# Optimization experiments

Measured on AMD Instinct MI355X. Metric: run time of the kernel, lower is better.

The kernel has to match this reference:

```python
import jax, jax.numpy as jnp
import numpy as np

K = 9
KS = (K - 1) // 2  # k_self
C_LIGHT = 299792458.0 / 1e6 / 600.0  # speed of light in detector units (as in HLayer)
BN_EPS = 1e-3  # keras BatchNormalization default epsilon


def _win2(f):
    # (B, N) -> (B, N, K): out[b, n, k] = f[b, n + k - KS], zero-padded at boundaries
    B, N = f.shape
    fp = jnp.pad(f, ((0, 0), (KS, KS)))
    return jnp.stack([fp[:, k:k + N] for k in range(K)], axis=2)


def _win3(f):
    # (B, N, F) -> (B, N, K, F): same shift-window along N
    B, N, F = f.shape
    fp = jnp.pad(f, ((0, 0), (KS, KS), (0, 0)))
    return jnp.stack([fp[:, k:k + N, :] for k in range(K)], axis=2)


def _valid_mask(N):
    # (N, K): True where neighbor index n + k - KS is in range
    idx = jnp.arange(N)[:, None] + jnp.arange(K)[None, :] - KS
    return (idx >= 0) & (idx < N)


def _hlayer(x):
    # x: (B, N, 6) with cols (t, c, a, px, py, pz) -> (B, N, K, 12)
    t, c, a = x[..., 0], x[..., 1], x[..., 2]
    px, py, pz = x[..., 3], x[..., 4], x[..., 5]
    N = x.shape[1]
    valid = _valid_mask(N)[None, :, :]  # (1, N, K)

    def d(f):  # shifted minus self, zeroed at boundaries (matches TF pad of the diff)
        return jnp.where(valid, _win2(f) - f[:, :, None], 0.0)

    dt, dx, dy, dz = d(t), d(px), d(py), d(pz)
    eu2 = dx * dx + dy * dy + dz * dz
    euclidean = jnp.sqrt(eu2)
    lorentz = (C_LIGHT * dt) ** 2 - eu2
    feats = [_win2(t), _win2(px), _win2(py), _win2(pz), _win2(c), _win2(a),
             dt, dx, dy, dz, euclidean, lorentz]
    return jnp.stack(feats, axis=3)  # (B, N, K, 12)


def _conv_bn(x, W, b, gamma, beta, mean, var):
    # kernel-size-1 Conv1D with relu activation, then inference-mode BatchNorm
    y = jax.nn.relu(jnp.matmul(x, W) + b)
    return gamma * (y - mean) * jax.lax.rsqrt(var + BN_EPS) + beta


def _make_params(key, dims):
    params = {}
    for i, (fi, fo) in enumerate(zip(dims[:-1], dims[1:])):
        key, k1 = jax.random.split(key)
        s = np.sqrt(2.0 / fi)
        params[f'W{i}'] = jax.random.normal(k1, (fi, fo), jnp.float32) * s
        params[f'b{i}'] = jnp.zeros((fo,), jnp.float32)
        key, k2, k3, k4 = jax.random.split(key, 4)
        params[f'g{i}'] = 1.0 + 0.1 * jax.random.normal(k2, (fo,), jnp.float32)
        params[f'be{i}'] = 0.1 * jax.random.normal(k3, (fo,), jnp.float32)
        params[f'mu{i}'] = 0.1 * jax.random.normal(k4, (fo,), jnp.float32)
        params[f'var{i}'] = 0.5 + jax.random.uniform(key, (fo,), jnp.float32)
    return params


def setup_inputs() -> dict:
    key = jax.random.key(0)
    kx, km, kf = jax.random.split(key, 3)
    B, N = 8, 4096
    x = jax.random.normal(kx, (B, N, 6), jnp.float32)
    dims_m = [12, 128, 256]   # MLayer/CRLayer stack on H features
    dims_f = [6, 128, 256]    # FRLayer stack on raw inputs
    pm = _make_params(km, dims_m)
    pf = _make_params(kf, dims_f)
    inp = {'x': x}
    for i in range(2):
        for n in ['W', 'b', 'g', 'be', 'mu', 'var']:
            inp[f'm_{n}{i}'] = pm[f'{n}{i}']
            inp[f'f_{n}{i}'] = pf[f'{n}{i}']
    return inp


def reference(x,
              m_W0, m_b0, m_g0, m_be0, m_mu0, m_var0,
              m_W1, m_b1, m_g1, m_be1, m_mu1, m_var1,
              f_W0, f_b0, f_g0, f_be0, f_mu0, f_var0,
              f_W1, f_b1, f_g1, f_be1, f_mu1, f_var1):
    # H-layer: (B, N, 6) -> (B, N, K, 12) geometric neighbor features
    h = _hlayer(x)
    # M branch (CRLayer, 1x1 convs over feature dim): -> m_nkf (B, N, K, 256)
    m = _conv_bn(h, m_W0, m_b0, m_g0, m_be0, m_mu0, m_var0)
    m = _conv_bn(m, m_W1, m_b1, m_g1, m_be1, m_mu1, m_var1)
    # FR branch on raw inputs: -> fr_nf (B, N, 256)
    fr = _conv_bn(x, f_W0, f_b0, f_g0, f_be0, f_mu0, f_var0)
    fr = _conv_bn(fr, f_W1, f_b1, f_g1, f_be1, f_mu1, f_var1)
    # A-layer: gate shifted fr by m and max-aggregate over K neighbors
    fr_sh = _win3(fr)                      # (B, N, K, 256), zero-padded shifts
    T = m * fr_sh                          # (B, N, K, 256)
    return jnp.max(T, axis=2)              # (B, N, 256)
```

## Files before the change

### kernel.cpp

```cpp
#include <hip/hip_runtime.h>
#include <hip/hip_bf16.h>

#define N_PTS 4096
#define C_LIGHT 0.49965409666666664f
#define BN_EPS 1e-3f

typedef __attribute__((ext_vector_type(8))) short short8;
typedef __attribute__((ext_vector_type(4))) float f32x4;

static __device__ __forceinline__ unsigned short f2bf(float f) {
    unsigned u = __float_as_uint(f);
    u += 0x7FFFu + ((u >> 16) & 1u);
    return (unsigned short)(u >> 16);
}
static __device__ __forceinline__ float bf2f(unsigned short h) {
    return __uint_as_float(((unsigned)h) << 16);
}
static __device__ __forceinline__ unsigned pk2(float a, float b) {
    __hip_bfloat162 h = __float22bfloat162_rn(make_float2(a, b));
    union { __hip_bfloat162 v; unsigned u; } cv;
    cv.v = h;
    return cv.u;
}

__global__ __launch_bounds__(256) void fold_kernel(
    const float* __restrict__ mW1, const float* __restrict__ mb1,
    const float* __restrict__ mg0, const float* __restrict__ mbe0,
    const float* __restrict__ mmu0, const float* __restrict__ mvar0,
    const float* __restrict__ mg1, const float* __restrict__ mbe1,
    const float* __restrict__ mmu1, const float* __restrict__ mvar1,
    const float* __restrict__ fW1p, const float* __restrict__ fb1,
    const float* __restrict__ fg0, const float* __restrict__ fbe0,
    const float* __restrict__ fmu0, const float* __restrict__ fvar0,
    const float* __restrict__ fg1, const float* __restrict__ fbe1,
    const float* __restrict__ fmu1, const float* __restrict__ fvar1,
    float* __restrict__ mBf, float* __restrict__ mS1, float* __restrict__ mT1,
    unsigned short* __restrict__ mWhi, unsigned short* __restrict__ mWlo,
    float* __restrict__ fBf, float* __restrict__ fS1, float* __restrict__ fT1,
    unsigned short* __restrict__ fWhi, unsigned short* __restrict__ fWlo)
{
    int br = blockIdx.x;
    const float* W1  = br ? fW1p : mW1;
    const float* b1  = br ? fb1  : mb1;
    const float* g0  = br ? fg0  : mg0;
    const float* be0 = br ? fbe0 : mbe0;
    const float* mu0 = br ? fmu0 : mmu0;
    const float* var0= br ? fvar0: mvar0;
    const float* g1  = br ? fg1  : mg1;
    const float* be1 = br ? fbe1 : mbe1;
    const float* mu1 = br ? fmu1 : mmu1;
    const float* var1= br ? fvar1: mvar1;
    float* Bf = br ? fBf : mBf;
    float* S1 = br ? fS1 : mS1;
    float* T1 = br ? fT1 : mT1;
    unsigned short* Whi = br ? fWhi : mWhi;
    unsigned short* Wlo = br ? fWlo : mWlo;

    __shared__ float s0s[128], t0s[128];
    int t = threadIdx.x;
    if (t < 128) {
        float s = g0[t] / sqrtf(var0[t] + BN_EPS);
        s0s[t] = s;
        t0s[t] = be0[t] - mu0[t] * s;
    }
    __syncthreads();

    {
        float s1 = g1[t] / sqrtf(var1[t] + BN_EPS);
        S1[t] = s1;
        T1[t] = be1[t] - mu1[t] * s1;
        float acc = b1[t];
        for (int i = 0; i < 128; ++i) acc = fmaf(t0s[i], W1[i * 256 + t], acc);
        Bf[t] = acc;
    }

    for (int e = t; e < 32768; e += 256) {
        int j = e & 7, l = (e >> 3) & 63, ks = (e >> 9) & 3, ct = e >> 11;
        int i = ks * 32 + (l >> 4) * 8 + j;
        int c = ct * 16 + (l & 15);
        float w = s0s[i] * W1[i * 256 + c];
        unsigned short hi = f2bf(w);
        unsigned short lo = f2bf(w - bf2f(hi));
        Whi[e] = hi;
        Wlo[e] = lo;
    }
}

__global__ __launch_bounds__(256, 2) void fr_kernel(
    const float* __restrict__ x,
    const float* __restrict__ W0,
    const float* __restrict__ b0,
    const short8* __restrict__ WfHi, const short8* __restrict__ WfLo,
    const float* __restrict__ Bf, const float* __restrict__ S1,
    const float* __restrict__ T1,
    float* __restrict__ frT)
{
    __shared__ float xs[64][6];
    __shared__ __attribute__((aligned(16))) float w0s[6][136];
    __shared__ __attribute__((aligned(16))) float b0s[128];
    __shared__ __attribute__((aligned(16))) unsigned short hAhi[4 * 64 * 8];
    __shared__ __attribute__((aligned(16))) unsigned short hAlo[4 * 64 * 8];

    int t = threadIdx.x;
    long row0 = (long)blockIdx.x * 64;

    for (int i = t; i < 384; i += 256) xs[i / 6][i % 6] = x[row0 * 6 + i];
    for (int i = t; i < 768; i += 256) w0s[i >> 7][i & 127] = W0[i];
    if (t < 128) b0s[t] = b0[t];

    int lane = t & 63, wv = t >> 6;
    int laneN = lane & 15, laneH = lane >> 4;
    int cg = t & 7;

    float bfv[4], s1v[4], t1v[4];
    int colc[4];
#pragma unroll
    for (int c = 0; c < 4; ++c) {
        colc[c] = (wv * 4 + c) * 16 + laneN;
        bfv[c] = Bf[colc[c]];
        s1v[c] = S1[colc[c]];
        t1v[c] = T1[colc[c]];
    }
    f32x4 acc[4][4];
#pragma unroll
    for (int mt = 0; mt < 4; ++mt)
#pragma unroll
        for (int c = 0; c < 4; ++c) {
            f32x4 z = {bfv[c], bfv[c], bfv[c], bfv[c]};
            acc[mt][c] = z;
        }
    __syncthreads();

    for (int ks = 0; ks < 4; ++ks) {
        int k0 = ks * 32 + cg * 4;
        float4 wreg[6];
#pragma unroll
        for (int i = 0; i < 6; ++i) wreg[i] = *(const float4*)&w0s[i][k0];
        float4 bq = *(const float4*)&b0s[k0];

        for (int idx = t; idx < 512; idx += 256) {
            int row = idx >> 3;
            float a0 = bq.x, a1 = bq.y, a2 = bq.z, a3 = bq.w;
#pragma unroll
            for (int i = 0; i < 6; ++i) {
                float hv = xs[row][i];
                a0 = fmaf(hv, wreg[i].x, a0);
                a1 = fmaf(hv, wreg[i].y, a1);
                a2 = fmaf(hv, wreg[i].z, a2);
                a3 = fmaf(hv, wreg[i].w, a3);
            }
            a0 = fmaxf(a0, 0.f); a1 = fmaxf(a1, 0.f);
            a2 = fmaxf(a2, 0.f); a3 = fmaxf(a3, 0.f);
            unsigned hi01 = pk2(a0, a1), hi23 = pk2(a2, a3);
            float q0 = __uint_as_float(hi01 << 16);
            float q1 = __uint_as_float(hi01 & 0xffff0000u);
            float q2 = __uint_as_float(hi23 << 16);
            float q3 = __uint_as_float(hi23 & 0xffff0000u);
            unsigned lo01 = pk2(a0 - q0, a1 - q1), lo23 = pk2(a2 - q2, a3 - q3);
            int mt = row >> 4, nl = row & 15;
            int base = (mt * 64 + (cg >> 1) * 16 + nl) * 8 + (cg & 1) * 4;
            *(uint2*)&hAhi[base] = make_uint2(hi01, hi23);
            *(uint2*)&hAlo[base] = make_uint2(lo01, lo23);
        }
        __syncthreads();

        short8 Bhi[4], Blo[4];
#pragma unroll
        for (int c = 0; c < 4; ++c) {
            int fo = ((wv * 4 + c) * 4 + ks) * 64 + lane;
            Bhi[c] = WfHi[fo];
            Blo[c] = WfLo[fo];
        }
#pragma unroll
        for (int mt = 0; mt < 4; ++mt) {
            short8 Ahi = *(const short8*)&hAhi[(mt * 64 + lane) * 8];
            short8 Alo = *(const short8*)&hAlo[(mt * 64 + lane) * 8];
#pragma unroll
            for (int c = 0; c < 4; ++c) {
                f32x4 a = acc[mt][c];
                a = __builtin_amdgcn_mfma_f32_16x16x32_bf16(Alo, Bhi[c], a, 0, 0, 0);
                a = __builtin_amdgcn_mfma_f32_16x16x32_bf16(Ahi, Blo[c], a, 0, 0, 0);
                a = __builtin_amdgcn_mfma_f32_16x16x32_bf16(Ahi, Bhi[c], a, 0, 0, 0);
                acc[mt][c] = a;
            }
        }
        __syncthreads();
    }

#pragma unroll
    for (int c = 0; c < 4; ++c)
#pragma unroll
        for (int mt = 0; mt < 4; ++mt) {
            float4 o;
            o.x = fmaf(fmaxf(acc[mt][c][0], 0.f), s1v[c], t1v[c]);
            o.y = fmaf(fmaxf(acc[mt][c][1], 0.f), s1v[c], t1v[c]);
            o.z = fmaf(fmaxf(acc[mt][c][2], 0.f), s1v[c], t1v[c]);
            o.w = fmaf(fmaxf(acc[mt][c][3], 0.f), s1v[c], t1v[c]);
            *(float4*)&frT[(long)colc[c] * 32768 + row0 + mt * 16 + laneH * 4] = o;
        }
}

#define SM_XS   0
#define SM_B0   576
#define SM_W0   1088
#define SM_HF   7616
#define SM_AHI  14528
#define SM_ALO  23744
#define SM_FRT  0
#define SM_OUT  33792
#define SM_TOT  50432

__global__ __launch_bounds__(256, 2) void fused_kernel(
    const float* __restrict__ x,
    const float* __restrict__ W0,
    const float* __restrict__ b0,
    const short8* __restrict__ WfHi, const short8* __restrict__ WfLo,
    const float* __restrict__ Bf, const float* __restrict__ S1,
    const float* __restrict__ T1,
    const float* __restrict__ frT,
    float* __restrict__ out)
{
    __shared__ __attribute__((aligned(16))) char smem[SM_TOT];
    float* xs  = (float*)(smem + SM_XS);
    float* b0s = (float*)(smem + SM_B0);
    float* w0s = (float*)(smem + SM_W0);
    float* hfp = (float*)(smem + SM_HF);
    unsigned short* hAhi = (unsigned short*)(smem + SM_AHI);
    unsigned short* hAlo = (unsigned short*)(smem + SM_ALO);
    float* frL = (float*)(smem + SM_FRT);
    float* oL  = (float*)(smem + SM_OUT);

    int t = threadIdx.x;
    int bn = blockIdx.x;
    int b  = bn >> 8;
    int n0 = (bn & 255) << 4;
    const float* xb = x + (long)b * N_PTS * 6;

    if (t < 144) {
        int rr = t / 6, cc = t % 6;
        int n = n0 - 4 + rr;
        xs[rr * 6 + cc] = (n >= 0 && n < N_PTS) ? xb[n * 6 + cc] : 0.f;
    }
    for (int i = t; i < 12 * 128; i += 256) w0s[(i >> 7) * 136 + (i & 127)] = W0[i];
    if (t < 128) b0s[t] = b0[t];
    __syncthreads();

    if (t < 144) {
        int kt = t >> 4, nl = t & 15;
        const float* self = &xs[(nl + 4) * 6];
        const float* nb   = &xs[(nl + kt) * 6];
        int nbn = n0 + nl + kt - 4;
        float msk = (nbn >= 0 && nbn < N_PTS) ? 1.f : 0.f;
        float dt = (nb[0] - self[0]) * msk;
        float dx = (nb[3] - self[3]) * msk;
        float dy = (nb[4] - self[4]) * msk;
        float dz = (nb[5] - self[5]) * msk;
        float eu2 = dx * dx + dy * dy + dz * dz;
        float* h = &hfp[t * 12];
        h[0]  = nb[0];
        h[1]  = nb[3];
        h[2]  = nb[4];
        h[3]  = nb[5];
        h[4]  = nb[1];
        h[5]  = nb[2];
        h[6]  = dt;
        h[7]  = dx;
        h[8]  = dy;
        h[9]  = dz;
        h[10] = sqrtf(eu2);
        float cdt = C_LIGHT * dt;
        h[11] = cdt * cdt - eu2;
    }

    int lane = t & 63, wv = t >> 6;
    int laneN = lane & 15, laneH = lane >> 4;
    int cg = t & 7;

    float bfv[4], s1v[4], t1v[4];
    int colc[4];
#pragma unroll
    for (int c = 0; c < 4; ++c) {
        colc[c] = (wv * 4 + c) * 16 + laneN;
        bfv[c] = Bf[colc[c]];
        s1v[c] = S1[colc[c]];
        t1v[c] = T1[colc[c]];
    }
    f32x4 acc[9][4];
#pragma unroll
    for (int kt = 0; kt < 9; ++kt)
#pragma unroll
        for (int c = 0; c < 4; ++c) {
            f32x4 z = {bfv[c], bfv[c], bfv[c], bfv[c]};
            acc[kt][c] = z;
        }
    __syncthreads();

    for (int ks = 0; ks < 4; ++ks) {
        int k0 = ks * 32 + cg * 4;
        float4 wreg[12];
#pragma unroll
        for (int i = 0; i < 12; ++i) wreg[i] = *(const float4*)&w0s[i * 136 + k0];
        float4 bq = *(const float4*)&b0s[k0];

        for (int idx = t; idx < 1152; idx += 256) {
            int row = idx >> 3;
            float a0 = bq.x, a1 = bq.y, a2 = bq.z, a3 = bq.w;
#pragma unroll
            for (int i = 0; i < 12; ++i) {
                float hv = hfp[row * 12 + i];
                a0 = fmaf(hv, wreg[i].x, a0);
                a1 = fmaf(hv, wreg[i].y, a1);
                a2 = fmaf(hv, wreg[i].z, a2);
                a3 = fmaf(hv, wreg[i].w, a3);
            }
            a0 = fmaxf(a0, 0.f); a1 = fmaxf(a1, 0.f);
            a2 = fmaxf(a2, 0.f); a3 = fmaxf(a3, 0.f);
            unsigned hi01 = pk2(a0, a1), hi23 = pk2(a2, a3);
            float q0 = __uint_as_float(hi01 << 16);
            float q1 = __uint_as_float(hi01 & 0xffff0000u);
            float q2 = __uint_as_float(hi23 << 16);
            float q3 = __uint_as_float(hi23 & 0xffff0000u);
            unsigned lo01 = pk2(a0 - q0, a1 - q1), lo23 = pk2(a2 - q2, a3 - q3);
            int kt = row >> 4, nl = row & 15;
            int base = (kt * 64 + (cg >> 1) * 16 + nl) * 8 + (cg & 1) * 4;
            *(uint2*)&hAhi[base] = make_uint2(hi01, hi23);
            *(uint2*)&hAlo[base] = make_uint2(lo01, lo23);
        }
        __syncthreads();

        short8 Bhi[4], Blo[4];
#pragma unroll
        for (int c = 0; c < 4; ++c) {
            int fo = ((wv * 4 + c) * 4 + ks) * 64 + lane;
            Bhi[c] = WfHi[fo];
            Blo[c] = WfLo[fo];
        }
#pragma unroll
        for (int kt = 0; kt < 9; ++kt) {
            short8 Ahi = *(const short8*)&hAhi[(kt * 64 + lane) * 8];
            short8 Alo = *(const short8*)&hAlo[(kt * 64 + lane) * 8];
#pragma unroll
            for (int c = 0; c < 4; ++c) {
                f32x4 a = acc[kt][c];
                a = __builtin_amdgcn_mfma_f32_16x16x32_bf16(Alo, Bhi[c], a, 0, 0, 0);
                a = __builtin_amdgcn_mfma_f32_16x16x32_bf16(Ahi, Blo[c], a, 0, 0, 0);
                a = __builtin_amdgcn_mfma_f32_16x16x32_bf16(Ahi, Bhi[c], a, 0, 0, 0);
                acc[kt][c] = a;
            }
        }
        __syncthreads();
    }
    for (int i = t; i < 2048; i += 256) {
        int col = i >> 3, seg = i & 7;
        int nn = n0 - 8 + seg * 4;
        float4 v = make_float4(0.f, 0.f, 0.f, 0.f);
        if (nn >= 0 && nn < N_PTS)
            v = *(const float4*)&frT[(long)col * 32768 + (b << 12) + nn];
        *(float4*)&frL[col * 33 + seg * 4] = v;
    }
    __syncthreads();

#pragma unroll
    for (int c = 0; c < 4; ++c) {
        float fv[12];
        int fb = colc[c] * 33 + laneH * 4 + 4;
#pragma unroll
        for (int j = 0; j < 12; ++j) fv[j] = frL[fb + j];
#pragma unroll
        for (int r = 0; r < 4; ++r) {
            float best;
#pragma unroll
            for (int kt = 0; kt < 9; ++kt) {
                float m = fmaf(fmaxf(acc[kt][c][r], 0.f), s1v[c], t1v[c]);
                float T = m * fv[r + kt];
                best = (kt == 0) ? T : fmaxf(best, T);
            }
            oL[(laneH * 4 + r) * 260 + colc[c]] = best;
        }
    }
    __syncthreads();

    float* outb = out + ((long)b << 20);
    for (int i = t; i < 1024; i += 256) {
        int row = i >> 6, c4 = (i & 63) << 2;
        float4 v = *(const float4*)&oL[row * 260 + c4];
        *(float4*)&outb[((long)(n0 + row) << 8) + c4] = v;
    }
}

extern "C" void kernel_launch(void* const* d_in, const int* in_sizes, int n_in,
                              void* d_out, int out_size, void* d_ws, size_t ws_size,
                              hipStream_t stream)
{
    const float* x = (const float*)d_in[0];
    const float* m_W0  = (const float*)d_in[1];
    const float* f_W0  = (const float*)d_in[2];
    const float* m_b0  = (const float*)d_in[3];
    const float* f_b0  = (const float*)d_in[4];
    const float* m_g0  = (const float*)d_in[5];
    const float* f_g0  = (const float*)d_in[6];
    const float* m_be0 = (const float*)d_in[7];
    const float* f_be0 = (const float*)d_in[8];
    const float* m_mu0 = (const float*)d_in[9];
    const float* f_mu0 = (const float*)d_in[10];
    const float* m_var0= (const float*)d_in[11];
    const float* f_var0= (const float*)d_in[12];
    const float* m_W1  = (const float*)d_in[13];
    const float* f_W1  = (const float*)d_in[14];
    const float* m_b1  = (const float*)d_in[15];
    const float* f_b1  = (const float*)d_in[16];
    const float* m_g1  = (const float*)d_in[17];
    const float* f_g1  = (const float*)d_in[18];
    const float* m_be1 = (const float*)d_in[19];
    const float* f_be1 = (const float*)d_in[20];
    const float* m_mu1 = (const float*)d_in[21];
    const float* f_mu1 = (const float*)d_in[22];
    const float* m_var1= (const float*)d_in[23];
    const float* f_var1= (const float*)d_in[24];

    char* wsb = (char*)d_ws;
    float* frT = (float*)wsb;
    float* mBf = (float*)(wsb + 33554432);
    float* mS1 = mBf + 256;
    float* mT1 = mS1 + 256;
    float* fBf = mT1 + 256;
    float* fS1 = fBf + 256;
    float* fT1 = fS1 + 256;
    unsigned short* mWhi = (unsigned short*)(fT1 + 256);
    unsigned short* mWlo = mWhi + 32768;
    unsigned short* fWhi = mWlo + 32768;
    unsigned short* fWlo = fWhi + 32768;

    fold_kernel<<<2, 256, 0, stream>>>(
        m_W1, m_b1, m_g0, m_be0, m_mu0, m_var0, m_g1, m_be1, m_mu1, m_var1,
        f_W1, f_b1, f_g0, f_be0, f_mu0, f_var0, f_g1, f_be1, f_mu1, f_var1,
        mBf, mS1, mT1, mWhi, mWlo,
        fBf, fS1, fT1, fWhi, fWlo);

    fr_kernel<<<8 * N_PTS / 64, 256, 0, stream>>>(
        x, f_W0, f_b0, (const short8*)fWhi, (const short8*)fWlo,
        fBf, fS1, fT1, frT);

    fused_kernel<<<8 * N_PTS / 16, 256, 0, stream>>>(
        x, m_W0, m_b0, (const short8*)mWhi, (const short8*)mWlo,
        mBf, mS1, mT1, frT, (float*)d_out);
}
```

Measured before the change: 239.6 us.

## Double-buffer hidden-layer fragments, store fr row-major, parallelize weight folding

Splits the weight-fold prep into a bias kernel plus a 32-block weight-fold kernel with vectorized stores, so that work is no longer done by just two blocks. fr_kernel now uses 32-row tiles with higher occupancy. It stages its output in LDS so it can write fr row-major (N×256) with coalesced float4 stores. Both fr_kernel and fused_kernel double-buffer the bf16 hi/lo A-fragments so the next K-slice's hidden layer is computed while the current MFMAs run, which drops one barrier per step. The fused kernel reads fr rows directly, but its LDS footprint grows to about 68KB, which may limit occupancy.

```diff
diff --git a/kernel.cpp b/kernel.cpp
--- a/kernel.cpp
+++ b/kernel.cpp
@@ -23,7 +23,7 @@
     return cv.u;
 }
 
-__global__ __launch_bounds__(256) void fold_kernel(
+__global__ __launch_bounds__(256) void fold_bias(
     const float* __restrict__ mW1, const float* __restrict__ mb1,
     const float* __restrict__ mg0, const float* __restrict__ mbe0,
     const float* __restrict__ mmu0, const float* __restrict__ mvar0,
@@ -35,9 +35,7 @@
     const float* __restrict__ fg1, const float* __restrict__ fbe1,
     const float* __restrict__ fmu1, const float* __restrict__ fvar1,
     float* __restrict__ mBf, float* __restrict__ mS1, float* __restrict__ mT1,
-    unsigned short* __restrict__ mWhi, unsigned short* __restrict__ mWlo,
-    float* __restrict__ fBf, float* __restrict__ fS1, float* __restrict__ fT1,
-    unsigned short* __restrict__ fWhi, unsigned short* __restrict__ fWlo)
+    float* __restrict__ fBf, float* __restrict__ fS1, float* __restrict__ fT1)
 {
     int br = blockIdx.x;
     const float* W1  = br ? fW1p : mW1;
@@ -53,64 +51,86 @@
     float* Bf = br ? fBf : mBf;
     float* S1 = br ? fS1 : mS1;
     float* T1 = br ? fT1 : mT1;
-    unsigned short* Whi = br ? fWhi : mWhi;
-    unsigned short* Wlo = br ? fWlo : mWlo;
-
-    __shared__ float s0s[128], t0s[128];
+
+    __shared__ float t0s[128];
     int t = threadIdx.x;
     if (t < 128) {
         float s = g0[t] / sqrtf(var0[t] + BN_EPS);
-        s0s[t] = s;
         t0s[t] = be0[t] - mu0[t] * s;
     }
     __syncthreads();
 
-    {
-        float s1 = g1[t] / sqrtf(var1[t] + BN_EPS);
-        S1[t] = s1;
-        T1[t] = be1[t] - mu1[t] * s1;
-        float acc = b1[t];
-        for (int i = 0; i < 128; ++i) acc = fmaf(t0s[i], W1[i * 256 + t], acc);
-        Bf[t] = acc;
-    }
-
-    for (int e = t; e < 32768; e += 256) {
-        int j = e & 7, l = (e >> 3) & 63, ks = (e >> 9) & 3, ct = e >> 11;
-        int i = ks * 32 + (l >> 4) * 8 + j;
-        int c = ct * 16 + (l & 15);
-        float w = s0s[i] * W1[i * 256 + c];
-        unsigned short hi = f2bf(w);
-        unsigned short lo = f2bf(w - bf2f(hi));
-        Whi[e] = hi;
-        Wlo[e] = lo;
-    }
-}
-
-__global__ __launch_bounds__(256, 2) void fr_kernel(
+    float s1 = g1[t] / sqrtf(var1[t] + BN_EPS);
+    S1[t] = s1;
+    T1[t] = be1[t] - mu1[t] * s1;
+    float acc = b1[t];
+    for (int i = 0; i < 128; ++i) acc = fmaf(t0s[i], W1[i * 256 + t], acc);
+    Bf[t] = acc;
+}
+
+__global__ __launch_bounds__(256) void fold_w(
+    const float* __restrict__ mW1,
+    const float* __restrict__ mg0, const float* __restrict__ mvar0,
+    const float* __restrict__ fW1p,
+    const float* __restrict__ fg0, const float* __restrict__ fvar0,
+    unsigned short* __restrict__ mWhi, unsigned short* __restrict__ mWlo,
+    unsigned short* __restrict__ fWhi, unsigned short* __restrict__ fWlo)
+{
+    int bid = blockIdx.x;
+    int br = bid >> 4, blk = bid & 15;
+    const float* W1  = br ? fW1p : mW1;
+    const float* g0  = br ? fg0  : mg0;
+    const float* var0= br ? fvar0: mvar0;
+    unsigned short* Whi = br ? fWhi : mWhi;
+    unsigned short* Wlo = br ? fWlo : mWlo;
+
+    __shared__ float s0s[128];
+    int t = threadIdx.x;
+    if (t < 128) s0s[t] = g0[t] / sqrtf(var0[t] + BN_EPS);
+    __syncthreads();
+
+    int e0 = blk * 2048 + t * 8;
+    int l = (e0 >> 3) & 63, ks = (e0 >> 9) & 3, ct = e0 >> 11;
+    int c = ct * 16 + (l & 15);
+    int ib = ks * 32 + (l >> 4) * 8;
+    unsigned short hi[8], lo[8];
+#pragma unroll
+    for (int j = 0; j < 8; ++j) {
+        float w = s0s[ib + j] * W1[(ib + j) * 256 + c];
+        hi[j] = f2bf(w);
+        lo[j] = f2bf(w - bf2f(hi[j]));
+    }
+    *(uint4*)&Whi[e0] = *(uint4*)hi;
+    *(uint4*)&Wlo[e0] = *(uint4*)lo;
+}
+
+__global__ __launch_bounds__(256, 3) void fr_kernel(
     const float* __restrict__ x,
     const float* __restrict__ W0,
     const float* __restrict__ b0,
     const short8* __restrict__ WfHi, const short8* __restrict__ WfLo,
     const float* __restrict__ Bf, const float* __restrict__ S1,
     const float* __restrict__ T1,
-    float* __restrict__ frT)
+    float* __restrict__ fr)
 {
-    __shared__ float xs[64][6];
+    __shared__ float xs[32][6];
     __shared__ __attribute__((aligned(16))) float w0s[6][136];
     __shared__ __attribute__((aligned(16))) float b0s[128];
-    __shared__ __attribute__((aligned(16))) unsigned short hAhi[4 * 64 * 8];
-    __shared__ __attribute__((aligned(16))) unsigned short hAlo[4 * 64 * 8];
+    __shared__ __attribute__((aligned(16))) unsigned short hAhi[2][1024];
+    __shared__ __attribute__((aligned(16))) unsigned short hAlo[2][1024];
+    __shared__ __attribute__((aligned(16))) float oL[32][260];
 
     int t = threadIdx.x;
-    long row0 = (long)blockIdx.x * 64;
-
-    for (int i = t; i < 384; i += 256) xs[i / 6][i % 6] = x[row0 * 6 + i];
+    long row0 = (long)blockIdx.x * 32;
+
+    if (t < 192) xs[t / 6][t % 6] = x[row0 * 6 + t];
     for (int i = t; i < 768; i += 256) w0s[i >> 7][i & 127] = W0[i];
     if (t < 128) b0s[t] = b0[t];
 
     int lane = t & 63, wv = t >> 6;
     int laneN = lane & 15, laneH = lane >> 4;
     int cg = t & 7;
+    int rowh = t >> 3;
 
     float bfv[4], s1v[4], t1v[4];
     int colc[4];
@@ -121,9 +141,9 @@
         s1v[c] = S1[colc[c]];
         t1v[c] = T1[colc[c]];
     }
-    f32x4 acc[4][4];
-#pragma unroll
-    for (int mt = 0; mt < 4; ++mt)
+    f32x4 acc[2][4];
+#pragma unroll
+    for (int mt = 0; mt < 2; ++mt)
 #pragma unroll
         for (int c = 0; c < 4; ++c) {
             f32x4 z = {bfv[c], bfv[c], bfv[c], bfv[c]};
@@ -131,39 +151,37 @@
         }
     __syncthreads();
 
+#define FR_HIDDEN(ks, bi)                                                     \
+    {                                                                         \
+        int k0 = (ks) * 32 + cg * 4;                                          \
+        float a0 = b0s[k0], a1 = b0s[k0+1], a2 = b0s[k0+2], a3 = b0s[k0+3];   \
+        _Pragma("unroll")                                                     \
+        for (int i = 0; i < 6; ++i) {                                         \
+            float hv = xs[rowh][i];                                           \
+            a0 = fmaf(hv, w0s[i][k0],   a0);                                  \
+            a1 = fmaf(hv, w0s[i][k0+1], a1);                                  \
+            a2 = fmaf(hv, w0s[i][k0+2], a2);                                  \
+            a3 = fmaf(hv, w0s[i][k0+3], a3);                                  \
+        }                                                                     \
+        a0 = fmaxf(a0, 0.f); a1 = fmaxf(a1, 0.f);                             \
+        a2 = fmaxf(a2, 0.f); a3 = fmaxf(a3, 0.f);                             \
+        unsigned hi01 = pk2(a0, a1), hi23 = pk2(a2, a3);                      \
+        float q0 = __uint_as_float(hi01 << 16);                               \
+        float q1 = __uint_as_float(hi01 & 0xffff0000u);                       \
+        float q2 = __uint_as_float(hi23 << 16);                               \
+        float q3 = __uint_as_float(hi23 & 0xffff0000u);                       \
+        unsigned lo01 = pk2(a0 - q0, a1 - q1), lo23 = pk2(a2 - q2, a3 - q3);  \
+        int mt = rowh >> 4, nl = rowh & 15;                                   \
+        int base = (mt * 64 + (cg >> 1) * 16 + nl) * 8 + (cg & 1) * 4;        \
+        *(uint2*)&hAhi[bi][base] = make_uint2(hi01, hi23);                    \
+        *(uint2*)&hAlo[bi][base] = make_uint2(lo01, lo23);                    \
+    }
+
+    FR_HIDDEN(0, 0)
+    __syncthreads();
+
     for (int ks = 0; ks < 4; ++ks) {
-        int k0 = ks * 32 + cg * 4;
-        float4 wreg[6];
-#pragma unroll
-        for (int i = 0; i < 6; ++i) wreg[i] = *(const float4*)&w0s[i][k0];
-        float4 bq = *(const float4*)&b0s[k0];
-
-        for (int idx = t; idx < 512; idx += 256) {
-            int row = idx >> 3;
-            float a0 = bq.x, a1 = bq.y, a2 = bq.z, a3 = bq.w;
-#pragma unroll
-            for (int i = 0; i < 6; ++i) {
-                float hv = xs[row][i];
-                a0 = fmaf(hv, wreg[i].x, a0);
-                a1 = fmaf(hv, wreg[i].y, a1);
-                a2 = fmaf(hv, wreg[i].z, a2);
-                a3 = fmaf(hv, wreg[i].w, a3);
-            }
-            a0 = fmaxf(a0, 0.f); a1 = fmaxf(a1, 0.f);
-            a2 = fmaxf(a2, 0.f); a3 = fmaxf(a3, 0.f);
-            unsigned hi01 = pk2(a0, a1), hi23 = pk2(a2, a3);
-            float q0 = __uint_as_float(hi01 << 16);
-            float q1 = __uint_as_float(hi01 & 0xffff0000u);
-            float q2 = __uint_as_float(hi23 << 16);
-            float q3 = __uint_as_float(hi23 & 0xffff0000u);
-            unsigned lo01 = pk2(a0 - q0, a1 - q1), lo23 = pk2(a2 - q2, a3 - q3);
-            int mt = row >> 4, nl = row & 15;
-            int base = (mt * 64 + (cg >> 1) * 16 + nl) * 8 + (cg & 1) * 4;
-            *(uint2*)&hAhi[base] = make_uint2(hi01, hi23);
-            *(uint2*)&hAlo[base] = make_uint2(lo01, lo23);
-        }
-        __syncthreads();
-
+        int bi = ks & 1;
         short8 Bhi[4], Blo[4];
 #pragma unroll
         for (int c = 0; c < 4; ++c) {
@@ -172,9 +190,9 @@
             Blo[c] = WfLo[fo];
         }
 #pragma unroll
-        for (int mt = 0; mt < 4; ++mt) {
-            short8 Ahi = *(const short8*)&hAhi[(mt * 64 + lane) * 8];
-            short8 Alo = *(const short8*)&hAlo[(mt * 64 + lane) * 8];
+        for (int mt = 0; mt < 2; ++mt) {
+            short8 Ahi = *(const short8*)&hAhi[bi][(mt * 64 + lane) * 8];
+            short8 Alo = *(const short8*)&hAlo[bi][(mt * 64 + lane) * 8];
 #pragma unroll
             for (int c = 0; c < 4; ++c) {
                 f32x4 a = acc[mt][c];
@@ -184,31 +202,35 @@
                 acc[mt][c] = a;
             }
         }
+        if (ks < 3) FR_HIDDEN(ks + 1, bi ^ 1)
         __syncthreads();
     }
 
 #pragma unroll
     for (int c = 0; c < 4; ++c)
 #pragma unroll
-        for (int mt = 0; mt < 4; ++mt) {
-            float4 o;
-            o.x = fmaf(fmaxf(acc[mt][c][0], 0.f), s1v[c], t1v[c]);
-            o.y = fmaf(fmaxf(acc[mt][c][1], 0.f), s1v[c], t1v[c]);
-            o.z = fmaf(fmaxf(acc[mt][c][2], 0.f), s1v[c], t1v[c]);
-            o.w = fmaf(fmaxf(acc[mt][c][3], 0.f), s1v[c], t1v[c]);
-            *(float4*)&frT[(long)colc[c] * 32768 + row0 + mt * 16 + laneH * 4] = o;
-        }
+        for (int mt = 0; mt < 2; ++mt)
+#pragma unroll
+            for (int r = 0; r < 4; ++r)
+                oL[mt * 16 + laneH * 4 + r][colc[c]] =
+                    fmaf(fmaxf(acc[mt][c][r], 0.f), s1v[c], t1v[c]);
+    __syncthreads();
+
+    for (int i = t; i < 2048; i += 256) {
+        int row = i >> 6, c4 = (i & 63) << 2;
+        float4 v = *(const float4*)&oL[row][c4];
+        *(float4*)&fr[(row0 + row) * 256 + c4] = v;
+    }
 }
 
 #define SM_XS   0
 #define SM_B0   576
 #define SM_W0   1088
 #define SM_HF   7616
-#define SM_AHI  14528
-#define SM_ALO  23744
-#define SM_FRT  0
-#define SM_OUT  33792
-#define SM_TOT  50432
+#define SM_FRAG 14528
+#define SM_FRL  14528
+#define SM_OUT  51392
+#define SM_TOT  68032
 
 __global__ __launch_bounds__(256, 2) void fused_kernel(
     const float* __restrict__ x,
@@ -217,7 +239,7 @@
     const short8* __restrict__ WfHi, const short8* __restrict__ WfLo,
     const float* __restrict__ Bf, const float* __restrict__ S1,
     const float* __restrict__ T1,
-    const float* __restrict__ frT,
+    const float* __restrict__ fr,
     float* __restrict__ out)
 {
     __shared__ __attribute__((aligned(16))) char smem[SM_TOT];
@@ -225,9 +247,7 @@
     float* b0s = (float*)(smem + SM_B0);
     float* w0s = (float*)(smem + SM_W0);
     float* hfp = (float*)(smem + SM_HF);
-    unsigned short* hAhi = (unsigned short*)(smem + SM_AHI);
-    unsigned short* hAlo = (unsigned short*)(smem + SM_ALO);
-    float* frL = (float*)(smem + SM_FRT);
+    float* frL = (float*)(smem + SM_FRL);
     float* oL  = (float*)(smem + SM_OUT);
 
     int t = threadIdx.x;
@@ -295,39 +315,48 @@
         }
     __syncthreads();
 
+#define FU_HIDDEN(ks, bi)                                                     \
+    {                                                                         \
+        unsigned short* Hhi = (unsigned short*)(smem + SM_FRAG) + (bi) * 9216;\
+        unsigned short* Hlo = Hhi + 4608;                                     \
+        int k0 = (ks) * 32 + cg * 4;                                          \
+        float4 wreg[12];                                                      \
+        _Pragma("unroll")                                                     \
+        for (int i = 0; i < 12; ++i) wreg[i] = *(const float4*)&w0s[i * 136 + k0]; \
+        float4 bq = *(const float4*)&b0s[k0];                                 \
+        for (int idx = t; idx < 1152; idx += 256) {                           \
+            int row = idx >> 3;                                               \
+            float a0 = bq.x, a1 = bq.y, a2 = bq.z, a3 = bq.w;                 \
+            _Pragma("unroll")                                                 \
+            for (int i = 0; i < 12; ++i) {                                    \
+                float hv = hfp[row * 12 + i];                                 \
+                a0 = fmaf(hv, wreg[i].x, a0);                                 \
+                a1 = fmaf(hv, wreg[i].y, a1);                                 \
+                a2 = fmaf(hv, wreg[i].z, a2);                                 \
+                a3 = fmaf(hv, wreg[i].w, a3);                                 \
+            }                                                                 \
+            a0 = fmaxf(a0, 0.f); a1 = fmaxf(a1, 0.f);                         \
+            a2 = fmaxf(a2, 0.f); a3 = fmaxf(a3, 0.f);                         \
+            unsigned hi01 = pk2(a0, a1), hi23 = pk2(a2, a3);                  \
+            float q0 = __uint_as_float(hi01 << 16);                           \
+            float q1 = __uint_as_float(hi01 & 0xffff0000u);                   \
+            float q2 = __uint_as_float(hi23 << 16);                           \
+            float q3 = __uint_as_float(hi23 & 0xffff0000u);                   \
+            unsigned lo01 = pk2(a0 - q0, a1 - q1), lo23 = pk2(a2 - q2, a3 - q3); \
+            int kt = row >> 4, nl = row & 15;                                 \
+            int base = (kt * 64 + (cg >> 1) * 16 + nl) * 8 + (cg & 1) * 4;    \
+            *(uint2*)&Hhi[base] = make_uint2(hi01, hi23);                     \
+            *(uint2*)&Hlo[base] = make_uint2(lo01, lo23);                     \
+        }                                                                     \
+    }
+
+    FU_HIDDEN(0, 0)
+    __syncthreads();
+
     for (int ks = 0; ks < 4; ++ks) {
-        int k0 = ks * 32 + cg * 4;
-        float4 wreg[12];
-#pragma unroll
-        for (int i = 0; i < 12; ++i) wreg[i] = *(const float4*)&w0s[i * 136 + k0];
-        float4 bq = *(const float4*)&b0s[k0];
-
-        for (int idx = t; idx < 1152; idx += 256) {
-            int row = idx >> 3;
-            float a0 = bq.x, a1 = bq.y, a2 = bq.z, a3 = bq.w;
-#pragma unroll
-            for (int i = 0; i < 12; ++i) {
-                float hv = hfp[row * 12 + i];
-                a0 = fmaf(hv, wreg[i].x, a0);
-                a1 = fmaf(hv, wreg[i].y, a1);
-                a2 = fmaf(hv, wreg[i].z, a2);
-                a3 = fmaf(hv, wreg[i].w, a3);
-            }
-            a0 = fmaxf(a0, 0.f); a1 = fmaxf(a1, 0.f);
-            a2 = fmaxf(a2, 0.f); a3 = fmaxf(a3, 0.f);
-            unsigned hi01 = pk2(a0, a1), hi23 = pk2(a2, a3);
-            float q0 = __uint_as_float(hi01 << 16);
-            float q1 = __uint_as_float(hi01 & 0xffff0000u);
-            float q2 = __uint_as_float(hi23 << 16);
-            float q3 = __uint_as_float(hi23 & 0xffff0000u);
-            unsigned lo01 = pk2(a0 - q0, a1 - q1), lo23 = pk2(a2 - q2, a3 - q3);
-            int kt = row >> 4, nl = row & 15;
-            int base = (kt * 64 + (cg >> 1) * 16 + nl) * 8 + (cg & 1) * 4;
-            *(uint2*)&hAhi[base] = make_uint2(hi01, hi23);
-            *(uint2*)&hAlo[base] = make_uint2(lo01, lo23);
-        }
-        __syncthreads();
-
+        int bi = ks & 1;
+        const unsigned short* Hhi = (const unsigned short*)(smem + SM_FRAG) + bi * 9216;
+        const unsigned short* Hlo = Hhi + 4608;
         short8 Bhi[4], Blo[4];
 #pragma unroll
         for (int c = 0; c < 4; ++c) {
@@ -337,8 +366,8 @@
         }
 #pragma unroll
         for (int kt = 0; kt < 9; ++kt) {
-            short8 Ahi = *(const short8*)&hAhi[(kt * 64 + lane) * 8];
-            short8 Alo = *(const short8*)&hAlo[(kt * 64 + lane) * 8];
+            short8 Ahi = *(const short8*)&Hhi[(kt * 64 + lane) * 8];
+            short8 Alo = *(const short8*)&Hlo[(kt * 64 + lane) * 8];
 #pragma unroll
             for (int c = 0; c < 4; ++c) {
                 f32x4 a = acc[kt][c];
@@ -348,24 +377,26 @@
                 acc[kt][c] = a;
             }
         }
+        if (ks < 3) FU_HIDDEN(ks + 1, bi ^ 1)
         __syncthreads();
     }
-    for (int i = t; i < 2048; i += 256) {
-        int col = i >> 3, seg = i & 7;
-        int nn = n0 - 8 + seg * 4;
+
+    for (int i = t; i < 1536; i += 256) {
+        int row = i >> 6, c4 = (i & 63) << 2;
+        int nn = n0 - 4 + row;
         float4 v = make_float4(0.f, 0.f, 0.f, 0.f);
         if (nn >= 0 && nn < N_PTS)
-            v = *(const float4*)&frT[(long)col * 32768 + (b << 12) + nn];
-        *(float4*)&frL[col * 33 + seg * 4] = v;
+            v = *(const float4*)&fr[(((long)(b << 12) + nn) << 8) + c4];
+        *(float4*)&frL[row * 260 + c4] = v;
     }
     __syncthreads();
 
 #pragma unroll
     for (int c = 0; c < 4; ++c) {
         float fv[12];
-        int fb = colc[c] * 33 + laneH * 4 + 4;
-#pragma unroll
-        for (int j = 0; j < 12; ++j) fv[j] = frL[fb + j];
+        int fb = (laneH * 4) * 260 + colc[c];
+#pragma unroll
+        for (int j = 0; j < 12; ++j) fv[j] = frL[fb + j * 260];
 #pragma unroll
         for (int r = 0; r < 4; ++r) {
             float best;
@@ -419,7 +450,7 @@
     const float* f_var1= (const float*)d_in[24];
 
     char* wsb = (char*)d_ws;
-    float* frT = (float*)wsb;
+    float* fr  = (float*)wsb;
     float* mBf = (float*)(wsb + 33554432);
     float* mS1 = mBf + 256;
     float* mT1 = mS1 + 256;
@@ -431,17 +462,20 @@
     unsigned short* fWhi = mWlo + 32768;
     unsigned short* fWlo = fWhi + 32768;
 
-    fold_kernel<<<2, 256, 0, stream>>>(
+    fold_bias<<<2, 256, 0, stream>>>(
         m_W1, m_b1, m_g0, m_be0, m_mu0, m_var0, m_g1, m_be1, m_mu1, m_var1,
         f_W1, f_b1, f_g0, f_be0, f_mu0, f_var0, f_g1, f_be1, f_mu1, f_var1,
-        mBf, mS1, mT1, mWhi, mWlo,
-        fBf, fS1, fT1, fWhi, fWlo);
-
-    fr_kernel<<<8 * N_PTS / 64, 256, 0, stream>>>(
+        mBf, mS1, mT1, fBf, fS1, fT1);
+
+    fold_w<<<32, 256, 0, stream>>>(
+        m_W1, m_g0, m_var0, f_W1, f_g0, f_var0,
+        mWhi, mWlo, fWhi, fWlo);
+
+    fr_kernel<<<8 * N_PTS / 32, 256, 0, stream>>>(
         x, f_W0, f_b0, (const short8*)fWhi, (const short8*)fWlo,
-        fBf, fS1, fT1, frT);
+        fBf, fS1, fT1, fr);
 
     fused_kernel<<<8 * N_PTS / 16, 256, 0, stream>>>(
         x, m_W0, m_b0, (const short8*)mWhi, (const short8*)mWlo,
-        mBf, mS1, mT1, frT, (float*)d_out);
-}
+        mBf, mS1, mT1, fr, (float*)d_out);
+}
```

After: 204.6 us. 14.6% less time.
